# Kernel optimization log

Measured on AMD Instinct MI355X. Metric: run time of the kernel, lower is better.

Reference implementation:

```python
import jax, jax.numpy as jnp
import numpy as np

N, E, F = 50000, 800000, 256
EPS = 1e-5


def _agg(h, src, dst, n):
    # gather src node features and sum into dst nodes (DGL copy_src + sum reduce)
    return jax.ops.segment_sum(h[src], dst, num_segments=n)


def _gcn_layer(h, src, dst, W, b):
    n = h.shape[0]
    h = _agg(h, src, dst, n)
    h = _agg(h, src, dst, n)  # update_all is called twice per layer
    return h @ W.T + b


def _batchnorm(h, gamma, beta):
    mean = jnp.mean(h, axis=0)
    var = jnp.mean(jnp.square(h - mean), axis=0)  # biased var, training mode
    return (h - mean) * jax.lax.rsqrt(var + EPS) * gamma + beta


def _branch(feature, src, dst, W1, b1, W2, b2, W3, b3, gamma, beta):
    h = _gcn_layer(feature, src, dst, W1, b1)
    h = _batchnorm(h, gamma, beta)
    h = _gcn_layer(h, src, dst, W2, b2)
    h = _gcn_layer(h, src, dst, W3, b3)
    return h


def setup_inputs() -> dict:
    key = jax.random.key(0)
    ks = jax.random.split(key, 12)
    s = 1.0 / np.sqrt(F)
    return {
        "feature": jax.random.normal(ks[0], (N, F), dtype=jnp.float32),
        "src1": jax.random.randint(ks[1], (E,), 0, N, dtype=jnp.int32),
        "dst1": jax.random.randint(ks[2], (E,), 0, N, dtype=jnp.int32),
        "src2": jax.random.randint(ks[3], (E,), 0, N, dtype=jnp.int32),
        "dst2": jax.random.randint(ks[4], (E,), 0, N, dtype=jnp.int32),
        "W1": jax.random.uniform(ks[5], (F, F), jnp.float32, -s, s),
        "b1": jax.random.uniform(ks[6], (F,), jnp.float32, -s, s),
        "W2": jax.random.uniform(ks[7], (F, F), jnp.float32, -s, s),
        "b2": jax.random.uniform(ks[8], (F,), jnp.float32, -s, s),
        "W3": jax.random.uniform(ks[9], (F, F), jnp.float32, -s, s),
        "b3": jax.random.uniform(ks[10], (F,), jnp.float32, -s, s),
        "gamma": jnp.ones((F,), jnp.float32),
        "beta": jnp.zeros((F,), jnp.float32),
    }


def reference(feature, src1, dst1, src2, dst2, W1, b1, W2, b2, W3, b3, gamma, beta):
    h1 = _branch(feature, src1, dst1, W1, b1, W2, b2, W3, b3, gamma, beta)
    h2 = _branch(feature, src2, dst2, W1, b1, W2, b2, W3, b3, gamma, beta)
    return h1.T @ h2  # [F, F]
```

## Files before the change

### kernel.cpp

```cpp
#include <hip/hip_runtime.h>
#include <hip/hip_fp16.h>

#define FDIM 256
#define GRAM_KS 192


__device__ __forceinline__ void h4acc(uint2 u, float4& a) {
  float2 f0 = __half22float2(*(__half2*)&u.x);
  float2 f1 = __half22float2(*(__half2*)&u.y);
  a.x += f0.x; a.y += f0.y; a.z += f1.x; a.w += f1.y;
}

__device__ __forceinline__ void h8f(uint4 u, float* f) {
  float2 t;
  t = __half22float2(*(__half2*)&u.x); f[0] = t.x; f[1] = t.y;
  t = __half22float2(*(__half2*)&u.y); f[2] = t.x; f[3] = t.y;
  t = __half22float2(*(__half2*)&u.z); f[4] = t.x; f[5] = t.y;
  t = __half22float2(*(__half2*)&u.w); f[6] = t.x; f[7] = t.y;
}

__global__ void k_hist(const int* __restrict__ dst, int* __restrict__ deg, int E) {
  int e = blockIdx.x * 256 + threadIdx.x;
  if (e < E) atomicAdd(&deg[dst[e]], 1);
}

__global__ __launch_bounds__(256) void k_blksum(const int* __restrict__ deg,
    int* __restrict__ blksum, int n) {
  int b = blockIdx.x, tid = threadIdx.x;
  int base = b * 1024 + tid * 4;
  int s = 0;
#pragma unroll
  for (int k = 0; k < 4; ++k) if (base + k < n) s += deg[base + k];
  for (int off = 32; off; off >>= 1) s += __shfl_down(s, off);
  __shared__ int ws4[4];
  if ((tid & 63) == 0) ws4[tid >> 6] = s;
  __syncthreads();
  if (tid == 0) blksum[b] = ws4[0] + ws4[1] + ws4[2] + ws4[3];
}

__global__ void k_blkscan(const int* __restrict__ blksum, int* __restrict__ blkoff, int nblk) {
  int lane = threadIdx.x;
  int carry = 0;
  for (int base = 0; base < nblk; base += 64) {
    int v = (base + lane < nblk) ? blksum[base + lane] : 0;
    int x = v;
    for (int off = 1; off < 64; off <<= 1) { int y = __shfl_up(x, off); if (lane >= off) x += y; }
    if (base + lane < nblk) blkoff[base + lane] = carry + x - v;
    carry += __shfl(x, 63);
  }
}

__global__ __launch_bounds__(256) void k_scan_blk(const int* __restrict__ deg,
    const int* __restrict__ blkoff, int* __restrict__ rowptr, int* __restrict__ cursor, int n) {
  int b = blockIdx.x, tid = threadIdx.x;
  int base = b * 1024 + tid * 4;
  int v[4];
#pragma unroll
  for (int k = 0; k < 4; ++k) v[k] = (base + k < n) ? deg[base + k] : 0;
  int s = v[0] + v[1] + v[2] + v[3];
  int lane = tid & 63, w = tid >> 6;
  int x = s;
  for (int off = 1; off < 64; off <<= 1) { int y = __shfl_up(x, off); if (lane >= off) x += y; }
  __shared__ int wsum[4];
  if (lane == 63) wsum[w] = x;
  __syncthreads();
  int wadd = 0;
  for (int i = 0; i < w; ++i) wadd += wsum[i];
  int run = blkoff[b] + wadd + x - s;
#pragma unroll
  for (int k = 0; k < 4; ++k) {
    if (base + k < n) { rowptr[base + k] = run; cursor[base + k] = run; }
    run += v[k];
  }
  if (n >= base && n <= base + 4) rowptr[n] = run;
}

__global__ void k_scatter(const int* __restrict__ src, const int* __restrict__ dst,
    int* __restrict__ cursor, int* __restrict__ esrc, int E) {
  int e = blockIdx.x * 256 + threadIdx.x;
  if (e < E) {
    int p = atomicAdd(&cursor[dst[e]], 1);
    esrc[p] = src[e];
  }
}

__global__ __launch_bounds__(256) void k_tr2(const float* __restrict__ W2,
    const float* __restrict__ W3, float* __restrict__ W2T, float* __restrict__ W3T) {
  __shared__ float tile[64][65];
  const float* src = blockIdx.z ? W3 : W2;
  float* dst = blockIdx.z ? W3T : W2T;
  int i0 = blockIdx.x * 64, j0 = blockIdx.y * 64;
  int tx = threadIdx.x & 63, ty = threadIdx.x >> 6;
#pragma unroll
  for (int m = 0; m < 16; ++m) {
    int r = ty * 16 + m;
    tile[r][tx] = src[(size_t)(i0 + r) * 256 + j0 + tx];
  }
  __syncthreads();
#pragma unroll
  for (int m = 0; m < 16; ++m) {
    int r = ty * 16 + m;
    dst[(size_t)(j0 + r) * 256 + i0 + tx] = tile[tx][r];
  }
}

__global__ __launch_bounds__(256) void k_f2h(const float* __restrict__ F,
    __half* __restrict__ H, int n4) {
  int i = blockIdx.x * 256 + threadIdx.x;
  if (i >= n4) return;
  float4 v = ((const float4*)F)[i];
  __half2 a = __floats2half2_rn(v.x, v.y);
  __half2 b = __floats2half2_rn(v.z, v.w);
  uint2 u; u.x = *(unsigned int*)&a; u.y = *(unsigned int*)&b;
  ((uint2*)H)[i] = u;
}

__global__ __launch_bounds__(256) void k_aggh(const __half* __restrict__ h,
    const int* __restrict__ rowptr, const int* __restrict__ esrc,
    __half* __restrict__ out, int n) {
  int wid = ((blockIdx.x * 256) + threadIdx.x) >> 6;
  int lane = threadIdx.x & 63;
  if (wid >= n) return;
  int beg = rowptr[wid], end = rowptr[wid + 1];
  const uint2* hv = (const uint2*)h;
  float4 a0 = {0,0,0,0}, a1 = {0,0,0,0}, a2 = {0,0,0,0}, a3 = {0,0,0,0};
  int e = beg;
  for (; e + 4 <= end; e += 4) {
    int s0 = esrc[e], s1 = esrc[e + 1], s2 = esrc[e + 2], s3 = esrc[e + 3];
    uint2 u0 = hv[(size_t)s0 * 64 + lane];
    uint2 u1 = hv[(size_t)s1 * 64 + lane];
    uint2 u2 = hv[(size_t)s2 * 64 + lane];
    uint2 u3 = hv[(size_t)s3 * 64 + lane];
    h4acc(u0, a0); h4acc(u1, a1); h4acc(u2, a2); h4acc(u3, a3);
  }
  for (; e < end; ++e) {
    uint2 u = hv[(size_t)esrc[e] * 64 + lane];
    h4acc(u, a0);
  }
  float4 r;
  r.x = ((a0.x + a1.x) + (a2.x + a3.x)) * 0.25f;
  r.y = ((a0.y + a1.y) + (a2.y + a3.y)) * 0.25f;
  r.z = ((a0.z + a1.z) + (a2.z + a3.z)) * 0.25f;
  r.w = ((a0.w + a1.w) + (a2.w + a3.w)) * 0.25f;
  __half2 ha = __floats2half2_rn(r.x, r.y);
  __half2 hb = __floats2half2_rn(r.z, r.w);
  uint2 uo; uo.x = *(unsigned int*)&ha; uo.y = *(unsigned int*)&hb;
  ((uint2*)out)[(size_t)wid * 64 + lane] = uo;
}

__global__ __launch_bounds__(256) void k_aggv2(const float* __restrict__ in1,
    const float* __restrict__ in2,
    const int* __restrict__ rp1, const int* __restrict__ es1,
    const int* __restrict__ rp2, const int* __restrict__ es2,
    float* __restrict__ out1, float* __restrict__ out2, int n, int useDeg) {
  int t = blockIdx.x * 256 + threadIdx.x;
  int g = t >> 4;
  int sl = t & 15;
  if (g >= 2 * n) return;
  int which = (g >= n) ? 1 : 0;
  int node = which ? g - n : g;
  const int* rp = which ? rp2 : rp1;
  const int* es = which ? es2 : es1;
  const float* in = which ? in2 : in1;
  float* out = which ? out2 : out1;
  int beg = rp[node], end = rp[node + 1];
  float s = 0.f;
  if (useDeg) {
    for (int e = beg + sl; e < end; e += 16) {
      int v = es[e];
      s += (float)(rp[v + 1] - rp[v]);
    }
  } else {
    for (int e = beg + sl; e < end; e += 16) s += in[es[e]];
  }
#pragma unroll
  for (int off = 8; off; off >>= 1) s += __shfl_down(s, off, 16);
  if (sl == 0) out[node] = s;
}

__global__ __launch_bounds__(256) void k_gram_sym(const __half* __restrict__ Xm,
    float* __restrict__ partial, int N, float* __restrict__ mc) {
  __shared__ float Xs[16][132];
  __shared__ float Ys[16][132];
  int tid = threadIdx.x;
  int t = blockIdx.x;
  int i0 = (t == 2) ? 128 : 0;
  int j0 = (t == 0) ? 0 : 128;
  bool diag = (t != 1);
  int z = blockIdx.z;
  int chunk = (N + GRAM_KS - 1) / GRAM_KS;
  int rb = z * chunk, re = min(N, rb + chunk);
  int lk = tid >> 4;
  int tj = tid & 15;
  int lc = tj * 8;
  int ti = lk;
  int cc = tid & 127, hh = tid >> 7;
  float xP = 0.f;
  float (*Yr)[132] = diag ? Xs : Ys;
  float acc[8][8] = {};
  for (int rr = rb; rr < re; rr += 16) {
    int r = rr + lk;
    float fx[8] = {}, fy[8] = {};
    if (r < re) {
      uint4 u = *(const uint4*)(Xm + (size_t)r * 256 + i0 + lc);
      h8f(u, fx);
      if (!diag) {
        uint4 v = *(const uint4*)(Xm + (size_t)r * 256 + j0 + lc);
        h8f(v, fy);
      }
    }
    *(float4*)&Xs[lk][lc] = *(float4*)&fx[0];
    *(float4*)&Xs[lk][lc + 4] = *(float4*)&fx[4];
    if (!diag) {
      *(float4*)&Ys[lk][lc] = *(float4*)&fy[0];
      *(float4*)&Ys[lk][lc + 4] = *(float4*)&fy[4];
    }
    __syncthreads();
    if (diag && mc) {
#pragma unroll
      for (int k = 0; k < 8; ++k) xP += Xs[hh * 8 + k][cc];
    }
#pragma unroll
    for (int k = 0; k < 16; ++k) {
      float av[8], bv[8];
      *(float4*)&av[0] = *(const float4*)&Xs[k][ti * 4];
      *(float4*)&av[4] = *(const float4*)&Xs[k][64 + ti * 4];
      *(float4*)&bv[0] = *(const float4*)&Yr[k][tj * 4];
      *(float4*)&bv[4] = *(const float4*)&Yr[k][64 + tj * 4];
#pragma unroll
      for (int i = 0; i < 8; ++i)
#pragma unroll
        for (int j = 0; j < 8; ++j) acc[i][j] += av[i] * bv[j];
    }
    __syncthreads();
  }
  float* pout = partial + (size_t)z * 65536;
#pragma unroll
  for (int i = 0; i < 8; ++i) {
    int row = i0 + ((i < 4) ? (ti * 4 + i) : (64 + ti * 4 + i - 4));
#pragma unroll
    for (int j = 0; j < 8; j += 4) {
      int col = j0 + ((j < 4) ? (tj * 4 + j) : (64 + tj * 4 + j - 4));
      *(float4*)(pout + (size_t)row * 256 + col) = *(float4*)&acc[i][j];
    }
  }
  if (diag && mc) {
    __syncthreads();
    Xs[hh][cc] = xP;
    __syncthreads();
    if (tid < 128) atomicAdd(&mc[i0 + tid], (Xs[0][tid] + Xs[1][tid]) * 16.0f);
  }
}

__global__ void k_gram_reduce_sym(const float* __restrict__ partial, float* __restrict__ C) {
  int idx = blockIdx.x * 256 + threadIdx.x;
  int i = idx >> 8, j = idx & 255;
  int sidx = (i >= 128 && j < 128) ? (j * 256 + i) : idx;
  float s = 0.f;
  for (int z = 0; z < GRAM_KS; ++z) s += partial[(size_t)z * 65536 + sidx];
  C[idx] = s * 256.0f;
}

__global__ __launch_bounds__(256) void k_gram(const __half* __restrict__ Xm,
    const __half* __restrict__ Ym, float* __restrict__ partial, int N,
    const float* __restrict__ wxA, const float* __restrict__ wxB, float* __restrict__ outX,
    const float* __restrict__ wyA, const float* __restrict__ wyB, float* __restrict__ outY) {
  __shared__ float Xs[16][132];
  __shared__ float Ys[16][132];
  __shared__ float wls[4][16];
  int tid = threadIdx.x;
  int i0 = blockIdx.x * 128, j0 = blockIdx.y * 128;
  int z = blockIdx.z;
  int chunk = (N + GRAM_KS - 1) / GRAM_KS;
  int rb = z * chunk, re = min(N, rb + chunk);
  int lk = tid >> 4;
  int tj = tid & 15;
  int lc = tj * 8;
  int ti = lk;
  bool doX = (outX != nullptr) && (blockIdx.y == 0);
  bool doY = (outY != nullptr) && (blockIdx.x == 0);
  int cc = tid & 127, hh = tid >> 7;
  float xA = 0, xB = 0, xP = 0, yA = 0, yB = 0, yP = 0;
  float acc[8][8] = {};
  for (int rr = rb; rr < re; rr += 16) {
    int r = rr + lk;
    float fx[8] = {}, fy[8] = {};
    if (r < re) {
      uint4 u = *(const uint4*)(Xm + (size_t)r * 256 + i0 + lc);
      uint4 v = *(const uint4*)(Ym + (size_t)r * 256 + j0 + lc);
      h8f(u, fx); h8f(v, fy);
    }
    *(float4*)&Xs[lk][lc] = *(float4*)&fx[0];
    *(float4*)&Xs[lk][lc + 4] = *(float4*)&fx[4];
    *(float4*)&Ys[lk][lc] = *(float4*)&fy[0];
    *(float4*)&Ys[lk][lc + 4] = *(float4*)&fy[4];
    if (tid < 64) {
      int grp = tid >> 4, kk = tid & 15, rw = rr + kk;
      const float* wp = (grp == 0) ? wxA : (grp == 1) ? wxB : (grp == 2) ? wyA : wyB;
      wls[grp][kk] = (wp && rw < re) ? wp[rw] : 0.f;
    }
    __syncthreads();
    if (doX) {
#pragma unroll
      for (int k = 0; k < 8; ++k) {
        float v = Xs[hh * 8 + k][cc];
        xP += v; xA += v * wls[0][hh * 8 + k]; xB += v * wls[1][hh * 8 + k];
      }
    }
    if (doY) {
#pragma unroll
      for (int k = 0; k < 8; ++k) {
        float v = Ys[hh * 8 + k][cc];
        yP += v; yA += v * wls[2][hh * 8 + k]; yB += v * wls[3][hh * 8 + k];
      }
    }
#pragma unroll
    for (int k = 0; k < 16; ++k) {
      float av[8], bv[8];
      *(float4*)&av[0] = *(const float4*)&Xs[k][ti * 4];
      *(float4*)&av[4] = *(const float4*)&Xs[k][64 + ti * 4];
      *(float4*)&bv[0] = *(const float4*)&Ys[k][tj * 4];
      *(float4*)&bv[4] = *(const float4*)&Ys[k][64 + tj * 4];
#pragma unroll
      for (int i = 0; i < 8; ++i)
#pragma unroll
        for (int j = 0; j < 8; ++j) acc[i][j] += av[i] * bv[j];
    }
    __syncthreads();
  }
  float* pout = partial + (size_t)z * 65536;
#pragma unroll
  for (int i = 0; i < 8; ++i) {
    int row = i0 + ((i < 4) ? (ti * 4 + i) : (64 + ti * 4 + i - 4));
#pragma unroll
    for (int j = 0; j < 8; j += 4) {
      int col = j0 + ((j < 4) ? (tj * 4 + j) : (64 + tj * 4 + j - 4));
      *(float4*)(pout + (size_t)row * 256 + col) = *(float4*)&acc[i][j];
    }
  }
  const float S6 = 4096.0f;
  if (doX) {
    __syncthreads();
    Xs[hh][cc] = xA;
    __syncthreads();
    if (tid < 128) atomicAdd(&outX[i0 + tid], (Xs[0][tid] + Xs[1][tid]) * S6);
    __syncthreads();
    Xs[hh][cc] = xB;
    __syncthreads();
    if (tid < 128) atomicAdd(&outX[256 + i0 + tid], (Xs[0][tid] + Xs[1][tid]) * S6);
    __syncthreads();
    Xs[hh][cc] = xP;
    __syncthreads();
    if (tid < 128) atomicAdd(&outX[512 + i0 + tid], (Xs[0][tid] + Xs[1][tid]) * S6);
  }
  if (doY) {
    __syncthreads();
    Ys[hh][cc] = yA;
    __syncthreads();
    if (tid < 128) atomicAdd(&outY[j0 + tid], (Ys[0][tid] + Ys[1][tid]) * S6);
    __syncthreads();
    Ys[hh][cc] = yB;
    __syncthreads();
    if (tid < 128) atomicAdd(&outY[256 + j0 + tid], (Ys[0][tid] + Ys[1][tid]) * S6);
    __syncthreads();
    Ys[hh][cc] = yP;
    __syncthreads();
    if (tid < 128) atomicAdd(&outY[512 + j0 + tid], (Ys[0][tid] + Ys[1][tid]) * S6);
  }
}

__global__ void k_gram_reduce(const float* __restrict__ partial, float* __restrict__ C) {
  int idx = blockIdx.x * 256 + threadIdx.x;
  float s = 0.f;
  for (int z = 0; z < GRAM_KS; ++z) s += partial[(size_t)z * 65536 + idx];
  C[idx] = s * 16777216.0f;
}

__global__ __launch_bounds__(256) void k_dots(const float* __restrict__ d1,
    const float* __restrict__ e1, const float* __restrict__ d2,
    const float* __restrict__ e2, float* scal, int n) {
  int i = blockIdx.x * 256 + threadIdx.x;
  float a = 0, b = 0, c = 0, d = 0;
  if (i < n) { a = d1[i]; b = e1[i]; c = d2[i]; d = e2[i]; }
  float v[8] = { b * d, b * c, b, a * d, a * c, a, d, c };
#pragma unroll
  for (int j = 0; j < 8; ++j) {
    float x = v[j];
    for (int off = 32; off; off >>= 1) x += __shfl_down(x, off);
    v[j] = x;
  }
  if ((threadIdx.x & 63) == 0)
#pragma unroll
    for (int j = 0; j < 8; ++j) atomicAdd(&scal[j], v[j]);
}

__global__ __launch_bounds__(256) void k_quad(const float* __restrict__ C,
    const float* __restrict__ W1, const float* __restrict__ m_raw,
    float* __restrict__ t, float* __restrict__ mv) {
  __shared__ float w[256];
  __shared__ float r1[256], r2[256];
  int j = blockIdx.x, tid = threadIdx.x;
  w[tid] = W1[j * 256 + tid];
  __syncthreads();
  float v = 0.f;
  for (int k = 0; k < 256; ++k) v += w[k] * C[k * 256 + tid];
  r1[tid] = v * w[tid];
  r2[tid] = w[tid] * m_raw[tid];
  __syncthreads();
  for (int off = 128; off; off >>= 1) {
    if (tid < off) { r1[tid] += r1[tid + off]; r2[tid] += r2[tid + off]; }
    __syncthreads();
  }
  if (tid == 0) { t[j] = r1[0]; mv[j] = r2[0]; }
}

__global__ __launch_bounds__(256) void k_bncoef(const float* __restrict__ t,
    const float* __restrict__ mv, const float* __restrict__ b1,
    const float* __restrict__ gamma, const float* __restrict__ beta,
    const float* __restrict__ W2T, const float* __restrict__ W3T,
    const float* __restrict__ b2, float* Dv, float* xv, float* yv, int n) {
  __shared__ float c[256], u[256];
  int j = threadIdx.x;
  float invn = 1.f / (float)n;
  float mean = mv[j] * invn + b1[j];
  float E2 = t[j] * invn + 2.f * b1[j] * mv[j] * invn + b1[j] * b1[j];
  float var = E2 - mean * mean;
  float D = gamma[j] * rsqrtf(var + 1e-5f);
  Dv[j] = D;
  c[j] = D * (b1[j] - mean) + beta[j];
  __syncthreads();
  float uu = 0.f;
  for (int k = 0; k < 256; ++k) uu += W2T[k * 256 + j] * c[k];
  u[j] = uu;
  __syncthreads();
  float xx = 0.f, yy = 0.f;
  for (int k = 0; k < 256; ++k) {
    xx += W3T[k * 256 + j] * u[k];
    yy += W3T[k * 256 + j] * b2[k];
  }
  xv[j] = xx;
  yv[j] = yy;
}

__global__ __launch_bounds__(256) void k_mm_small(float* __restrict__ Cm,
    const float* __restrict__ A, const float* __restrict__ B,
    const float* __restrict__ s, int transA) {
  __shared__ float a[256];
  int i = blockIdx.x, j = threadIdx.x;
  float av = transA ? A[j * 256 + i] : A[i * 256 + j];
  a[j] = s ? av * s[j] : av;
  __syncthreads();
  float acc = 0.f;
  for (int k = 0; k < 256; ++k) acc += a[k] * B[k * 256 + j];
  Cm[i * 256 + j] = acc;
}

__global__ __launch_bounds__(256) void k_mv6(const float* __restrict__ R1,
    const float* __restrict__ R2, const float* __restrict__ pX,
    const float* __restrict__ qY, float* __restrict__ vout) {
  __shared__ float w[256];
  int b = blockIdx.x, j = threadIdx.x;
  const float* M = (b < 3) ? R1 : R2;
  const float* wv = (b < 3) ? (pX + b * 256) : (qY + (b - 3) * 256);
  w[j] = wv[j];
  __syncthreads();
  float s = 0.f;
  for (int k = 0; k < 256; ++k) s += M[k * 256 + j] * w[k];
  vout[b * 256 + j] = s;
}

__global__ __launch_bounds__(256) void k_mm_final(float* __restrict__ out,
    const float* __restrict__ R1, const float* __restrict__ T1,
    const float* __restrict__ vout,
    const float* __restrict__ x1, const float* __restrict__ x2,
    const float* __restrict__ yv, const float* __restrict__ b3,
    const float* __restrict__ scal, float fN) {
  __shared__ float a[256];
  int i = blockIdx.x, j = threadIdx.x;
  a[j] = R1[j * 256 + i];
  __syncthreads();
  float acc = 0.f;
  for (int k = 0; k < 256; ++k) acc += a[k] * T1[k * 256 + j];
  float s1 = scal[0] * x2[j] + scal[1] * yv[j] + scal[2] * b3[j];
  float s2 = scal[3] * x2[j] + scal[4] * yv[j] + scal[5] * b3[j];
  float s3 = scal[6] * x2[j] + scal[7] * yv[j] + fN * b3[j];
  acc += vout[i] * x2[j] + vout[256 + i] * yv[j] + vout[512 + i] * b3[j];
  acc += x1[i] * (vout[768 + j] + s1) + yv[i] * (vout[1024 + j] + s2)
       + b3[i] * (vout[1280 + j] + s3);
  out[i * 256 + j] = acc;
}

extern "C" void kernel_launch(void* const* d_in, const int* in_sizes, int n_in,
                              void* d_out, int out_size, void* d_ws, size_t ws_size,
                              hipStream_t stream) {
  const float* feature = (const float*)d_in[0];
  const int* src1 = (const int*)d_in[1];
  const int* dst1 = (const int*)d_in[2];
  const int* src2 = (const int*)d_in[3];
  const int* dst2 = (const int*)d_in[4];
  const float* W1 = (const float*)d_in[5];
  const float* b1 = (const float*)d_in[6];
  const float* W2 = (const float*)d_in[7];
  const float* b2 = (const float*)d_in[8];
  const float* W3 = (const float*)d_in[9];
  const float* b3 = (const float*)d_in[10];
  const float* gamma = (const float*)d_in[11];
  const float* beta = (const float*)d_in[12];
  const int N = in_sizes[0] / FDIM;
  const int E = in_sizes[1];
  float* out = (float*)d_out;

  size_t NF = (size_t)N * FDIM;
  __half* FH = (__half*)d_ws;
  __half* Xh = FH + NF;
  __half* Yh = Xh + NF;
  __half* G2A = Yh + NF;
  float* partial = (float*)(G2A + NF);
  int* rowptr1 = (int*)(partial + (size_t)GRAM_KS * 65536);
  int* rowptr2 = rowptr1 + (N + 1);
  int* cursor = rowptr2 + (N + 1);
  int* esrc1 = cursor + N;
  int* esrc2 = esrc1 + E;
  float* vtmp1 = (float*)(esrc2 + E);
  float* vtmp2 = vtmp1 + N;
  float* d1 = vtmp2 + N; float* e1 = d1 + N; float* d2 = e1 + N; float* e2 = d2 + N;
  float* C = e2 + N;
  float* mcA = C + 65536;
  float* mcB = mcA + 256;
  float* pX = mcB + 256;
  float* qY = pX + 768;
  float* scal = qY + 768;
  float* tq = scal + 16; float* mv = tq + 256;
  float* Dv = mv + 256; float* x1 = Dv + 256; float* x2 = x1 + 256; float* yv = x2 + 256;
  float* Q = yv + 256; float* R1 = Q + 65536; float* R2 = R1 + 65536;
  float* Z = R2 + 65536; float* T1 = Z + 65536;
  float* W2T = T1 + 65536; float* W3T = W2T + 65536;
  float* vout = W3T + 65536;
  int* blksum = (int*)(vout + 1536);
  int* blkoff = blksum + 1024;

  const int eb = (E + 255) / 256;
  const int nb = (N + 255) / 256;
  const int aggb = (N + 3) / 4;
  const int avb2 = (2 * N * 16 + 255) / 256;
  const int nblk = (N + 1023) / 1024;

  auto build = [&](const int* s_, const int* d_, int* rp, int* es) {
    hipMemsetAsync(cursor, 0, (size_t)N * sizeof(int), stream);
    k_hist<<<eb, 256, 0, stream>>>(d_, cursor, E);
    k_blksum<<<nblk, 256, 0, stream>>>(cursor, blksum, N);
    k_blkscan<<<1, 64, 0, stream>>>(blksum, blkoff, nblk);
    k_scan_blk<<<nblk, 256, 0, stream>>>(cursor, blkoff, rp, cursor, N);
    k_scatter<<<eb, 256, 0, stream>>>(s_, d_, cursor, es, E);
  };

  k_tr2<<<dim3(4, 4, 2), 256, 0, stream>>>(W2, W3, W2T, W3T);
  k_f2h<<<(int)((NF / 4 + 255) / 256), 256, 0, stream>>>(feature, FH, (int)(NF / 4));
  build(src1, dst1, rowptr1, esrc1);
  build(src2, dst2, rowptr2, esrc2);
  hipMemsetAsync(mcA, 0, (256 * 2 + 768 * 2 + 16) * sizeof(float), stream);

  k_aggv2<<<avb2, 256, 0, stream>>>(nullptr, nullptr, rowptr1, esrc1, rowptr2, esrc2,
                                    d1, d2, N, 1);
  k_aggv2<<<avb2, 256, 0, stream>>>(d1, d2, rowptr1, esrc1, rowptr2, esrc2,
                                    vtmp1, vtmp2, N, 0);
  k_aggv2<<<avb2, 256, 0, stream>>>(vtmp1, vtmp2, rowptr1, esrc1, rowptr2, esrc2,
                                    e1, e2, N, 0);
  k_dots<<<nb, 256, 0, stream>>>(d1, e1, d2, e2, scal, N);

  auto do_branch = [&](const int* rp, const int* es, __half* G2dst,
                       float* mc, float* xvec, float* Rdst) {
    k_aggh<<<aggb, 256, 0, stream>>>(FH, rp, es, Xh, N);
    k_aggh<<<aggb, 256, 0, stream>>>(Xh, rp, es, Yh, N);
    k_gram_sym<<<dim3(3, 1, GRAM_KS), 256, 0, stream>>>(Yh, partial, N, mc);
    k_gram_reduce_sym<<<256, 256, 0, stream>>>(partial, C);
    k_quad<<<256, 256, 0, stream>>>(C, W1, mc, tq, mv);
    k_bncoef<<<1, 256, 0, stream>>>(tq, mv, b1, gamma, beta, W2T, W3T, b2, Dv, xvec, yv, N);
    k_mm_small<<<256, 256, 0, stream>>>(Q, W1, W2T, Dv, 1);
    k_mm_small<<<256, 256, 0, stream>>>(Rdst, Q, W3T, nullptr, 0);
    k_aggh<<<aggb, 256, 0, stream>>>(Yh, rp, es, Xh, N);
    k_aggh<<<aggb, 256, 0, stream>>>(Xh, rp, es, Yh, N);
    k_aggh<<<aggb, 256, 0, stream>>>(Yh, rp, es, Xh, N);
    k_aggh<<<aggb, 256, 0, stream>>>(Xh, rp, es, G2dst, N);
  };

  do_branch(rowptr1, esrc1, G2A, mcA, x1, R1);
  do_branch(rowptr2, esrc2, Yh, mcB, x2, R2);

  k_gram<<<dim3(2, 2, GRAM_KS), 256, 0, stream>>>(G2A, Yh, partial, N,
      e2, d2, pX, e1, d1, qY);
  k_gram_reduce<<<256, 256, 0, stream>>>(partial, Z);

  k_mm_small<<<256, 256, 0, stream>>>(T1, Z, R2, nullptr, 0);
  k_mv6<<<6, 256, 0, stream>>>(R1, R2, pX, qY, vout);
  k_mm_final<<<256, 256, 0, stream>>>(out, R1, T1, vout, x1, x2, yv, b3, scal, (float)N);
}
```

Before: 1.562 ms.

## Use MFMA fp16 matrix cores for Gram partial products

Rewrites both Gram kernels so they keep fp16 tiles transposed in LDS and compute the 128x128 block products with mfma_f32_16x16x32_f16 instructions instead of scalar fp32 FMAs. The K step grows from 16 to 32 rows per iteration, and the column-sum and weighted-sum side reductions are adapted to the new LDS layout. The goal is to cut the FMA-bound cost of the Gram stage. The price is a more complex LDS transpose step and uncoalesced scalar stores of the partial sums.

New measurement: 1.370 ms. 12.3% less time.

```diff
diff --git a/kernel.cpp b/kernel.cpp
--- a/kernel.cpp
+++ b/kernel.cpp
@@ -4,19 +4,23 @@
 #define FDIM 256
 #define GRAM_KS 192
 
+
+typedef _Float16 f16x8 __attribute__((ext_vector_type(8)));
+typedef float f32x4 __attribute__((ext_vector_type(4)));
+
+union H8 { uint2 u2[2]; f16x8 v; };
+
+__device__ __forceinline__ f16x8 ldfrag(const __half* ldsT, int m, int g) {
+  H8 h;
+  h.u2[0] = *(const uint2*)(ldsT + m * 36 + g * 4);
+  h.u2[1] = *(const uint2*)(ldsT + m * 36 + 16 + g * 4);
+  return h.v;
+}
 
 __device__ __forceinline__ void h4acc(uint2 u, float4& a) {
   float2 f0 = __half22float2(*(__half2*)&u.x);
   float2 f1 = __half22float2(*(__half2*)&u.y);
   a.x += f0.x; a.y += f0.y; a.z += f1.x; a.w += f1.y;
-}
-
-__device__ __forceinline__ void h8f(uint4 u, float* f) {
-  float2 t;
-  t = __half22float2(*(__half2*)&u.x); f[0] = t.x; f[1] = t.y;
-  t = __half22float2(*(__half2*)&u.y); f[2] = t.x; f[3] = t.y;
-  t = __half22float2(*(__half2*)&u.z); f[4] = t.x; f[5] = t.y;
-  t = __half22float2(*(__half2*)&u.w); f[6] = t.x; f[7] = t.y;
 }
 
 __global__ void k_hist(const int* __restrict__ dst, int* __restrict__ deg, int E) {
@@ -180,8 +184,8 @@
 
 __global__ __launch_bounds__(256) void k_gram_sym(const __half* __restrict__ Xm,
     float* __restrict__ partial, int N, float* __restrict__ mc) {
-  __shared__ float Xs[16][132];
-  __shared__ float Ys[16][132];
+  __shared__ __half ldsA[128 * 36];
+  __shared__ __half ldsB[128 * 36];
   int tid = threadIdx.x;
   int t = blockIdx.x;
   int i0 = (t == 2) ? 128 : 0;
@@ -190,65 +194,76 @@
   int z = blockIdx.z;
   int chunk = (N + GRAM_KS - 1) / GRAM_KS;
   int rb = z * chunk, re = min(N, rb + chunk);
-  int lk = tid >> 4;
-  int tj = tid & 15;
-  int lc = tj * 8;
-  int ti = lk;
+  int lane = tid & 63, w = tid >> 6;
+  int g = lane >> 4;
+  int lm = lane & 15;
+  int wm = w >> 1, wn = w & 1;
+  int sp = tid >> 4;
+  int sc = (tid & 15) * 8;
   int cc = tid & 127, hh = tid >> 7;
   float xP = 0.f;
-  float (*Yr)[132] = diag ? Xs : Ys;
-  float acc[8][8] = {};
-  for (int rr = rb; rr < re; rr += 16) {
-    int r = rr + lk;
-    float fx[8] = {}, fy[8] = {};
-    if (r < re) {
-      uint4 u = *(const uint4*)(Xm + (size_t)r * 256 + i0 + lc);
-      h8f(u, fx);
-      if (!diag) {
-        uint4 v = *(const uint4*)(Xm + (size_t)r * 256 + j0 + lc);
-        h8f(v, fy);
+  f32x4 acc[4][4] = {};
+  const __half* Bsrc = diag ? ldsA : ldsB;
+  for (int rr = rb; rr < re; rr += 32) {
+    int r0 = rr + 2 * sp, r1 = r0 + 1;
+    uint4 a0 = {0,0,0,0}, a1 = {0,0,0,0}, b0 = {0,0,0,0}, b1 = {0,0,0,0};
+    if (r0 < re) a0 = *(const uint4*)(Xm + (size_t)r0 * 256 + i0 + sc);
+    if (r1 < re) a1 = *(const uint4*)(Xm + (size_t)r1 * 256 + i0 + sc);
+    if (!diag) {
+      if (r0 < re) b0 = *(const uint4*)(Xm + (size_t)r0 * 256 + j0 + sc);
+      if (r1 < re) b1 = *(const uint4*)(Xm + (size_t)r1 * 256 + j0 + sc);
+    }
+    __syncthreads();
+    {
+      const unsigned short* pa0 = (const unsigned short*)&a0;
+      const unsigned short* pa1 = (const unsigned short*)&a1;
+      const unsigned short* pb0 = (const unsigned short*)&b0;
+      const unsigned short* pb1 = (const unsigned short*)&b1;
+#pragma unroll
+      for (int j = 0; j < 8; ++j) {
+        *(unsigned int*)(ldsA + (sc + j) * 36 + 2 * sp) =
+            (unsigned int)pa0[j] | ((unsigned int)pa1[j] << 16);
+        if (!diag)
+          *(unsigned int*)(ldsB + (sc + j) * 36 + 2 * sp) =
+              (unsigned int)pb0[j] | ((unsigned int)pb1[j] << 16);
       }
     }
-    *(float4*)&Xs[lk][lc] = *(float4*)&fx[0];
-    *(float4*)&Xs[lk][lc + 4] = *(float4*)&fx[4];
-    if (!diag) {
-      *(float4*)&Ys[lk][lc] = *(float4*)&fy[0];
-      *(float4*)&Ys[lk][lc + 4] = *(float4*)&fy[4];
-    }
     __syncthreads();
     if (diag && mc) {
-#pragma unroll
-      for (int k = 0; k < 8; ++k) xP += Xs[hh * 8 + k][cc];
-    }
-#pragma unroll
-    for (int k = 0; k < 16; ++k) {
-      float av[8], bv[8];
-      *(float4*)&av[0] = *(const float4*)&Xs[k][ti * 4];
-      *(float4*)&av[4] = *(const float4*)&Xs[k][64 + ti * 4];
-      *(float4*)&bv[0] = *(const float4*)&Yr[k][tj * 4];
-      *(float4*)&bv[4] = *(const float4*)&Yr[k][64 + tj * 4];
-#pragma unroll
-      for (int i = 0; i < 8; ++i)
-#pragma unroll
-        for (int j = 0; j < 8; ++j) acc[i][j] += av[i] * bv[j];
-    }
-    __syncthreads();
+      const __half* p = ldsA + cc * 36 + hh * 16;
+#pragma unroll
+      for (int k = 0; k < 16; ++k) xP += __half2float(p[k]);
+    }
+    f16x8 af[4];
+#pragma unroll
+    for (int fm = 0; fm < 4; ++fm) af[fm] = ldfrag(ldsA, wm * 64 + fm * 16 + lm, g);
+#pragma unroll
+    for (int fn = 0; fn < 4; ++fn) {
+      f16x8 bf = ldfrag(Bsrc, wn * 64 + fn * 16 + lm, g);
+#pragma unroll
+      for (int fm = 0; fm < 4; ++fm)
+        acc[fm][fn] = __builtin_amdgcn_mfma_f32_16x16x32_f16(af[fm], bf, acc[fm][fn], 0, 0, 0);
+    }
   }
   float* pout = partial + (size_t)z * 65536;
 #pragma unroll
-  for (int i = 0; i < 8; ++i) {
-    int row = i0 + ((i < 4) ? (ti * 4 + i) : (64 + ti * 4 + i - 4));
-#pragma unroll
-    for (int j = 0; j < 8; j += 4) {
-      int col = j0 + ((j < 4) ? (tj * 4 + j) : (64 + tj * 4 + j - 4));
-      *(float4*)(pout + (size_t)row * 256 + col) = *(float4*)&acc[i][j];
+  for (int fm = 0; fm < 4; ++fm) {
+#pragma unroll
+    for (int reg = 0; reg < 4; ++reg) {
+      int row = i0 + wm * 64 + fm * 16 + g * 4 + reg;
+#pragma unroll
+      for (int fn = 0; fn < 4; ++fn) {
+        int col = j0 + wn * 64 + fn * 16 + lm;
+        pout[(size_t)row * 256 + col] = acc[fm][fn][reg];
+      }
     }
   }
   if (diag && mc) {
     __syncthreads();
-    Xs[hh][cc] = xP;
-    __syncthreads();
-    if (tid < 128) atomicAdd(&mc[i0 + tid], (Xs[0][tid] + Xs[1][tid]) * 16.0f);
+    float* fs = (float*)ldsA;
+    fs[hh * 128 + cc] = xP;
+    __syncthreads();
+    if (tid < 128) atomicAdd(&mc[i0 + tid], (fs[tid] + fs[128 + tid]) * 16.0f);
   }
 }
 
@@ -265,107 +280,125 @@
     const __half* __restrict__ Ym, float* __restrict__ partial, int N,
     const float* __restrict__ wxA, const float* __restrict__ wxB, float* __restrict__ outX,
     const float* __restrict__ wyA, const float* __restrict__ wyB, float* __restrict__ outY) {
-  __shared__ float Xs[16][132];
-  __shared__ float Ys[16][132];
-  __shared__ float wls[4][16];
+  __shared__ __half ldsA[128 * 36];
+  __shared__ __half ldsB[128 * 36];
+  __shared__ float wls[4][32];
   int tid = threadIdx.x;
   int i0 = blockIdx.x * 128, j0 = blockIdx.y * 128;
   int z = blockIdx.z;
   int chunk = (N + GRAM_KS - 1) / GRAM_KS;
   int rb = z * chunk, re = min(N, rb + chunk);
-  int lk = tid >> 4;
-  int tj = tid & 15;
-  int lc = tj * 8;
-  int ti = lk;
+  int lane = tid & 63, w = tid >> 6;
+  int g = lane >> 4;
+  int lm = lane & 15;
+  int wm = w >> 1, wn = w & 1;
+  int sp = tid >> 4;
+  int sc = (tid & 15) * 8;
   bool doX = (outX != nullptr) && (blockIdx.y == 0);
   bool doY = (outY != nullptr) && (blockIdx.x == 0);
   int cc = tid & 127, hh = tid >> 7;
   float xA = 0, xB = 0, xP = 0, yA = 0, yB = 0, yP = 0;
-  float acc[8][8] = {};
-  for (int rr = rb; rr < re; rr += 16) {
-    int r = rr + lk;
-    float fx[8] = {}, fy[8] = {};
-    if (r < re) {
-      uint4 u = *(const uint4*)(Xm + (size_t)r * 256 + i0 + lc);
-      uint4 v = *(const uint4*)(Ym + (size_t)r * 256 + j0 + lc);
-      h8f(u, fx); h8f(v, fy);
-    }
-    *(float4*)&Xs[lk][lc] = *(float4*)&fx[0];
-    *(float4*)&Xs[lk][lc + 4] = *(float4*)&fx[4];
-    *(float4*)&Ys[lk][lc] = *(float4*)&fy[0];
-    *(float4*)&Ys[lk][lc + 4] = *(float4*)&fy[4];
-    if (tid < 64) {
-      int grp = tid >> 4, kk = tid & 15, rw = rr + kk;
+  f32x4 acc[4][4] = {};
+  for (int rr = rb; rr < re; rr += 32) {
+    int r0 = rr + 2 * sp, r1 = r0 + 1;
+    uint4 a0 = {0,0,0,0}, a1 = {0,0,0,0}, b0 = {0,0,0,0}, b1 = {0,0,0,0};
+    if (r0 < re) {
+      a0 = *(const uint4*)(Xm + (size_t)r0 * 256 + i0 + sc);
+      b0 = *(const uint4*)(Ym + (size_t)r0 * 256 + j0 + sc);
+    }
+    if (r1 < re) {
+      a1 = *(const uint4*)(Xm + (size_t)r1 * 256 + i0 + sc);
+      b1 = *(const uint4*)(Ym + (size_t)r1 * 256 + j0 + sc);
+    }
+    __syncthreads();
+    {
+      const unsigned short* pa0 = (const unsigned short*)&a0;
+      const unsigned short* pa1 = (const unsigned short*)&a1;
+      const unsigned short* pb0 = (const unsigned short*)&b0;
+      const unsigned short* pb1 = (const unsigned short*)&b1;
+#pragma unroll
+      for (int j = 0; j < 8; ++j) {
+        *(unsigned int*)(ldsA + (sc + j) * 36 + 2 * sp) =
+            (unsigned int)pa0[j] | ((unsigned int)pa1[j] << 16);
+        *(unsigned int*)(ldsB + (sc + j) * 36 + 2 * sp) =
+            (unsigned int)pb0[j] | ((unsigned int)pb1[j] << 16);
+      }
+    }
+    if (tid < 128) {
+      int grp = tid >> 5, kk = tid & 31, rw = rr + kk;
       const float* wp = (grp == 0) ? wxA : (grp == 1) ? wxB : (grp == 2) ? wyA : wyB;
       wls[grp][kk] = (wp && rw < re) ? wp[rw] : 0.f;
     }
     __syncthreads();
     if (doX) {
-#pragma unroll
-      for (int k = 0; k < 8; ++k) {
-        float v = Xs[hh * 8 + k][cc];
-        xP += v; xA += v * wls[0][hh * 8 + k]; xB += v * wls[1][hh * 8 + k];
+      const __half* p = ldsA + cc * 36 + hh * 16;
+#pragma unroll
+      for (int k = 0; k < 16; ++k) {
+        float v = __half2float(p[k]);
+        xP += v; xA += v * wls[0][hh * 16 + k]; xB += v * wls[1][hh * 16 + k];
       }
     }
     if (doY) {
-#pragma unroll
-      for (int k = 0; k < 8; ++k) {
-        float v = Ys[hh * 8 + k][cc];
-        yP += v; yA += v * wls[2][hh * 8 + k]; yB += v * wls[3][hh * 8 + k];
+      const __half* p = ldsB + cc * 36 + hh * 16;
+#pragma unroll
+      for (int k = 0; k < 16; ++k) {
+        float v = __half2float(p[k]);
+        yP += v; yA += v * wls[2][hh * 16 + k]; yB += v * wls[3][hh * 16 + k];
       }
     }
-#pragma unroll
-    for (int k = 0; k < 16; ++k) {
-      float av[8], bv[8];
-      *(float4*)&av[0] = *(const float4*)&Xs[k][ti * 4];
-      *(float4*)&av[4] = *(const float4*)&Xs[k][64 + ti * 4];
-      *(float4*)&bv[0] = *(const float4*)&Ys[k][tj * 4];
-      *(float4*)&bv[4] = *(const float4*)&Ys[k][64 + tj * 4];
-#pragma unroll
-      for (int i = 0; i < 8; ++i)
-#pragma unroll
-        for (int j = 0; j < 8; ++j) acc[i][j] += av[i] * bv[j];
-    }
-    __syncthreads();
+    f16x8 af[4];
+#pragma unroll
+    for (int fm = 0; fm < 4; ++fm) af[fm] = ldfrag(ldsA, wm * 64 + fm * 16 + lm, g);
+#pragma unroll
+    for (int fn = 0; fn < 4; ++fn) {
+      f16x8 bf = ldfrag(ldsB, wn * 64 + fn * 16 + lm, g);
+#pragma unroll
+      for (int fm = 0; fm < 4; ++fm)
+        acc[fm][fn] = __builtin_amdgcn_mfma_f32_16x16x32_f16(af[fm], bf, acc[fm][fn], 0, 0, 0);
+    }
   }
   float* pout = partial + (size_t)z * 65536;
 #pragma unroll
-  for (int i = 0; i < 8; ++i) {
-    int row = i0 + ((i < 4) ? (ti * 4 + i) : (64 + ti * 4 + i - 4));
-#pragma unroll
-    for (int j = 0; j < 8; j += 4) {
-      int col = j0 + ((j < 4) ? (tj * 4 + j) : (64 + tj * 4 + j - 4));
-      *(float4*)(pout + (size_t)row * 256 + col) = *(float4*)&acc[i][j];
+  for (int fm = 0; fm < 4; ++fm) {
+#pragma unroll
+    for (int reg = 0; reg < 4; ++reg) {
+      int row = i0 + wm * 64 + fm * 16 + g * 4 + reg;
+#pragma unroll
+      for (int fn = 0; fn < 4; ++fn) {
+        int col = j0 + wn * 64 + fn * 16 + lm;
+        pout[(size_t)row * 256 + col] = acc[fm][fn][reg];
+      }
     }
   }
   const float S6 = 4096.0f;
+  float* fs = (float*)ldsA;
   if (doX) {
     __syncthreads();
-    Xs[hh][cc] = xA;
-    __syncthreads();
-    if (tid < 128) atomicAdd(&outX[i0 + tid], (Xs[0][tid] + Xs[1][tid]) * S6);
-    __syncthreads();
-    Xs[hh][cc] = xB;
-    __syncthreads();
-    if (tid < 128) atomicAdd(&outX[256 + i0 + tid], (Xs[0][tid] + Xs[1][tid]) * S6);
-    __syncthreads();
-    Xs[hh][cc] = xP;
-    __syncthreads();
-    if (tid < 128) atomicAdd(&outX[512 + i0 + tid], (Xs[0][tid] + Xs[1][tid]) * S6);
+    fs[hh * 128 + cc] = xA;
+    __syncthreads();
+    if (tid < 128) atomicAdd(&outX[i0 + tid], (fs[tid] + fs[128 + tid]) * S6);
+    __syncthreads();
+    fs[hh * 128 + cc] = xB;
+    __syncthreads();
+    if (tid < 128) atomicAdd(&outX[256 + i0 + tid], (fs[tid] + fs[128 + tid]) * S6);
+    __syncthreads();
+    fs[hh * 128 + cc] = xP;
+    __syncthreads();
+    if (tid < 128) atomicAdd(&outX[512 + i0 + tid], (fs[tid] + fs[128 + tid]) * S6);
   }
   if (doY) {
     __syncthreads();
-    Ys[hh][cc] = yA;
-    __syncthreads();
-    if (tid < 128) atomicAdd(&outY[j0 + tid], (Ys[0][tid] + Ys[1][tid]) * S6);
-    __syncthreads();
-    Ys[hh][cc] = yB;
-    __syncthreads();
-    if (tid < 128) atomicAdd(&outY[256 + j0 + tid], (Ys[0][tid] + Ys[1][tid]) * S6);
-    __syncthreads();
-    Ys[hh][cc] = yP;
-    __syncthreads();
-    if (tid < 128) atomicAdd(&outY[512 + j0 + tid], (Ys[0][tid] + Ys[1][tid]) * S6);
+    fs[hh * 128 + cc] = yA;
+    __syncthreads();
+    if (tid < 128) atomicAdd(&outY[j0 + tid], (fs[tid] + fs[128 + tid]) * S6);
+    __syncthreads();
+    fs[hh * 128 + cc] = yB;
+    __syncthreads();
+    if (tid < 128) atomicAdd(&outY[256 + j0 + tid], (fs[tid] + fs[128 + tid]) * S6);
+    __syncthreads();
+    fs[hh * 128 + cc] = yP;
+    __syncthreads();
+    if (tid < 128) atomicAdd(&outY[512 + j0 + tid], (fs[tid] + fs[128 + tid]) * S6);
   }
 }
 
```
